# Performance work log

Measured on AMD Instinct MI355X. Metric: run time of the kernel, lower is better.

Reference implementation:

```python
import jax, jax.numpy as jnp
import numpy as np

EMBED_DIM = 768
NUM_HEADS = 12
HEAD_DIM = EMBED_DIM // NUM_HEADS


def setup_inputs() -> dict:
    key = jax.random.key(0)
    ks = jax.random.split(key, 12)
    B, T, D, Hp, Wp = 4, 32, EMBED_DIM, 16, 16
    h = jax.random.normal(ks[0], (B, T, D, Hp, Wp), dtype=jnp.float32)
    u_enc = jax.random.uniform(ks[1], (B, T, D, Hp, Wp), dtype=jnp.float32)
    lam = jax.random.uniform(ks[2], (B, T, 1, Hp, Wp), dtype=jnp.float32)
    s = 1.0 / np.sqrt(D)
    Wq = jax.random.normal(ks[3], (D, D), dtype=jnp.float32) * s
    bq = jnp.zeros((D,), dtype=jnp.float32)
    Wk = jax.random.normal(ks[4], (D, D), dtype=jnp.float32) * s
    bk = jnp.zeros((D,), dtype=jnp.float32)
    Wv = jax.random.normal(ks[5], (D, D), dtype=jnp.float32) * s
    bv = jnp.zeros((D,), dtype=jnp.float32)
    Wo = jax.random.normal(ks[6], (D, D), dtype=jnp.float32) * s
    bo = jnp.zeros((D,), dtype=jnp.float32)
    return {"h": h, "u_enc": u_enc, "lam": lam,
            "Wq": Wq, "bq": bq, "Wk": Wk, "bk": bk,
            "Wv": Wv, "bv": bv, "Wo": Wo, "bo": bo}


def reference(h, u_enc, lam, Wq, bq, Wk, bk, Wv, bv, Wo, bo):
    B, T, D, Hp, Wp = h.shape
    S = Hp * Wp
    NH, HD = NUM_HEADS, HEAD_DIM
    # (B,T,D,Hp,Wp) -> (B*S, T, D)
    h_seq = jnp.transpose(h, (0, 3, 4, 1, 2)).reshape(B * S, T, D)
    u_seq = jnp.transpose(u_enc, (0, 3, 4, 1, 2)).reshape(B * S, T, D)
    lam_seq = jnp.transpose(lam, (0, 3, 4, 1, 2)).reshape(B * S, T)
    # projections (nn.Linear: x @ W.T + b)
    Q = (h_seq @ Wq.T + bq).reshape(B * S, T, NH, HD).transpose(0, 2, 1, 3)
    K = (h_seq @ Wk.T + bk).reshape(B * S, T, NH, HD).transpose(0, 2, 1, 3)
    V = (h_seq @ Wv.T + bv).reshape(B * S, T, NH, HD).transpose(0, 2, 1, 3)
    scores = jnp.einsum('bhqd,bhkd->bhqk', Q, K) / jnp.sqrt(jnp.float32(HD))
    # key-dependent uncertainty penalty: lam_j * mean_d(u_j)
    u_pen = lam_seq * u_seq.mean(axis=-1)  # (B*S, T)
    scores = scores - u_pen[:, None, None, :]
    attn = jax.nn.softmax(scores, axis=-1)  # dropout: eval mode (identity)
    out = jnp.einsum('bhqk,bhkd->bhqd', attn, V)
    out = out.transpose(0, 2, 1, 3).reshape(B * S, T, D)
    out = out @ Wo.T + bo
    return jnp.transpose(out.reshape(B, Hp, Wp, T, D), (0, 3, 4, 1, 2))
```

## Files before the change

### kernel.cpp

```cpp
#include <hip/hip_runtime.h>

typedef float   f32x4 __attribute__((ext_vector_type(4)));
typedef _Float16 f16x8 __attribute__((ext_vector_type(8)));

#define DEV static __device__ __forceinline__

#define BB 4
#define TT 32
#define DD 768
#define SS 256
#define NHD 12
#define HD 64
#define NSEQ  (BB*SS)
#define MTOK  (NSEQ*TT)

DEV void async_copy16(const _Float16* g, _Float16* l) {
  __builtin_amdgcn_global_load_lds(
      (const __attribute__((address_space(1))) unsigned int*)g,
      (__attribute__((address_space(3))) unsigned int*)l,
      16, 0, 0);
}

DEV int swz_chunk(int r, int kc) {
  return r * 4 + (kc ^ (r & 3) ^ ((r >> 2) & 3));
}

__global__ __launch_bounds__(256) void k_transpose_h(const float* __restrict__ h,
                                                     _Float16* __restrict__ A) {
  __shared__ _Float16 Tl[256 * 65];
  const int slab = blockIdx.x;
  const int d0   = blockIdx.y * 64;
  const int t    = threadIdx.x;
  const float4* hv = (const float4*)(h + (slab * DD + d0) * SS);
  #pragma unroll
  for (int i = 0; i < 16; ++i) {
    int dd = i * 4 + (t >> 6);
    int s4 = (t & 63) * 4;
    float4 v = hv[dd * 64 + (t & 63)];
    Tl[(s4 + 0) * 65 + dd] = (_Float16)v.x;
    Tl[(s4 + 1) * 65 + dd] = (_Float16)v.y;
    Tl[(s4 + 2) * 65 + dd] = (_Float16)v.z;
    Tl[(s4 + 3) * 65 + dd] = (_Float16)v.w;
  }
  __syncthreads();
  #pragma unroll
  for (int p = 0; p < 8; ++p) {
    int s  = p * 32 + (t >> 3);
    int dd = (t & 7) * 8;
    f16x8 val;
    #pragma unroll
    for (int j = 0; j < 8; ++j) val[j] = Tl[s * 65 + dd + j];
    *(f16x8*)(A + (slab * SS + s) * DD + d0 + dd) = val;
  }
}

__global__ __launch_bounds__(256) void k_convert_w(const float* __restrict__ Wq,
                                                   const float* __restrict__ Wk,
                                                   const float* __restrict__ Wv,
                                                   const float* __restrict__ Wo,
                                                   _Float16* __restrict__ WQKV,
                                                   _Float16* __restrict__ WoH) {
  int idx = blockIdx.x * 256 + threadIdx.x;
  int row = idx / 96;
  int c8  = (idx % 96) * 8;
  const float* src; _Float16* dst;
  if (row < 768)       { src = Wq + row * 768;          dst = WQKV + row * 768; }
  else if (row < 1536) { src = Wk + (row - 768) * 768;  dst = WQKV + row * 768; }
  else if (row < 2304) { src = Wv + (row - 1536) * 768; dst = WQKV + row * 768; }
  else                 { src = Wo + (row - 2304) * 768; dst = WoH  + (row - 2304) * 768; }
  float4 v0 = *(const float4*)(src + c8);
  float4 v1 = *(const float4*)(src + c8 + 4);
  f16x8 o;
  o[0]=(_Float16)v0.x; o[1]=(_Float16)v0.y; o[2]=(_Float16)v0.z; o[3]=(_Float16)v0.w;
  o[4]=(_Float16)v1.x; o[5]=(_Float16)v1.y; o[6]=(_Float16)v1.z; o[7]=(_Float16)v1.w;
  *(f16x8*)(dst + c8) = o;
}

__global__ __launch_bounds__(256) void k_upen(const float* __restrict__ u,
                                              const float* __restrict__ lam,
                                              float* __restrict__ upen) {
  int slab = blockIdx.x >> 2;
  int q    = blockIdx.x & 3;
  int s    = threadIdx.x;
  const float* base = u + (slab * DD + q * 192) * SS + s;
  float sum = 0.f;
  for (int d = 0; d < 192; ++d) sum += base[d * SS];
  int b = slab >> 5, tt = slab & 31;
  float l = lam[slab * SS + s];
  atomicAdd(&upen[(b * SS + s) * TT + tt], sum * l * (1.0f / 768.0f));
}

__global__ __launch_bounds__(512, 2) void k_gemm_qkv(const _Float16* __restrict__ A,
                                                     const _Float16* __restrict__ Bw,
                                                     const float* __restrict__ bq,
                                                     const float* __restrict__ bk,
                                                     const float* __restrict__ bv,
                                                     _Float16* __restrict__ Qp,
                                                     _Float16* __restrict__ Kp,
                                                     _Float16* __restrict__ Vp) {
  __shared__ __align__(16) _Float16 As[2][256 * 64];
  __shared__ __align__(16) _Float16 Bs[2][256 * 64];
  const int swz = (blockIdx.x & 7) * 144 + (blockIdx.x >> 3);
  const int mt = swz / 9, nt = swz - mt * 9;
  const int m0 = mt * 256, n0 = nt * 256;
  const int tid = threadIdx.x, lane = tid & 63, w = tid >> 6;
  const int wm = w >> 2, wn = w & 3;
  f32x4 acc[8][4] = {};

  auto stage = [&](const _Float16* __restrict__ g, int grow0, _Float16* l, int k0) {
    #pragma unroll
    for (int li = 0; li < 4; ++li) {
      int cc = tid + 512 * li;
      int row = cc >> 3;
      int kc = (cc & 7) ^ (row & 7);
      async_copy16(g + (grow0 + row) * DD + k0 + kc * 8, l + cc * 8);
    }
  };

  stage(A, m0, &As[0][0], 0);
  stage(Bw, n0, &Bs[0][0], 0);
  __syncthreads();

  for (int it = 0; it < 12; ++it) {
    const int cb = it & 1;
    const _Float16* Ac = &As[cb][0];
    const _Float16* Bc = &Bs[cb][0];
    const int kn = (it + 1) * 64;
    f16x8 bfr[4][2];
    #pragma unroll
    for (int p = 0; p < 4; ++p) {
      f16x8 afr[2][2];
      #pragma unroll
      for (int q = 0; q < 2; ++q)
        #pragma unroll
        for (int kk = 0; kk < 2; ++kk) {
          int row = wm * 128 + (2 * p + q) * 16 + (lane & 15);
          int kc = kk * 4 + (lane >> 4);
          afr[q][kk] = *(const f16x8*)&Ac[row * 64 + (kc ^ (row & 7)) * 8];
        }
      if (p == 0) {
        #pragma unroll
        for (int ni = 0; ni < 4; ++ni)
          #pragma unroll
          for (int kk = 0; kk < 2; ++kk) {
            int row = wn * 64 + ni * 16 + (lane & 15);
            int kc = kk * 4 + (lane >> 4);
            bfr[ni][kk] = *(const f16x8*)&Bc[row * 64 + (kc ^ (row & 7)) * 8];
          }
        if (it < 11) stage(A, m0, &As[cb ^ 1][0], kn);
      }
      if (p == 1 && it < 11) stage(Bw, n0, &Bs[cb ^ 1][0], kn);
      __builtin_amdgcn_s_barrier();
      asm volatile("s_waitcnt lgkmcnt(0)" ::: "memory");
      __builtin_amdgcn_sched_barrier(0);
      __builtin_amdgcn_s_setprio(1);
      #pragma unroll
      for (int q = 0; q < 2; ++q)
        #pragma unroll
        for (int ni = 0; ni < 4; ++ni) {
          acc[2 * p + q][ni] = __builtin_amdgcn_mfma_f32_16x16x32_f16(
              afr[q][0], bfr[ni][0], acc[2 * p + q][ni], 0, 0, 0);
          acc[2 * p + q][ni] = __builtin_amdgcn_mfma_f32_16x16x32_f16(
              afr[q][1], bfr[ni][1], acc[2 * p + q][ni], 0, 0, 0);
        }
      __builtin_amdgcn_s_setprio(0);
      __builtin_amdgcn_s_barrier();
    }
    asm volatile("s_waitcnt vmcnt(0)" ::: "memory");
    __builtin_amdgcn_sched_barrier(0);
    __builtin_amdgcn_s_barrier();
  }

  const int sel = nt / 3;
  const float scale = (sel == 0) ? 0.125f : 1.0f;
  const float* bias = (sel == 0) ? bq : ((sel == 1) ? bk : bv);
  _Float16* dst = (sel == 0) ? Qp : ((sel == 1) ? Kp : Vp);
  const int b = mt >> 5, t = mt & 31;
  #pragma unroll
  for (int ni = 0; ni < 4; ++ni) {
    int n768 = nt * 256 - sel * 768 + wn * 64 + ni * 16 + (lane & 15);
    int head = n768 >> 6, hd = n768 & 63;
    float bs = bias[n768];
    long hb = (long)head * 2048 + t * 64 + hd;
    #pragma unroll
    for (int mi = 0; mi < 8; ++mi) {
      f32x4 v = acc[mi][ni];
      #pragma unroll
      for (int r = 0; r < 4; ++r) {
        int s = wm * 128 + mi * 16 + (lane >> 4) * 4 + r;
        long seq = (long)b * 256 + s;
        dst[seq * 24576 + hb] = (_Float16)((v[r] + bs) * scale);
      }
    }
  }
}

__global__ __launch_bounds__(256) void k_attn(const _Float16* __restrict__ Qp,
                                              const _Float16* __restrict__ Kp,
                                              const _Float16* __restrict__ Vp,
                                              const float* __restrict__ upen,
                                              _Float16* __restrict__ O) {
  __shared__ _Float16 lds[4][32 * 66 + 32 * 40];
  const int w = threadIdx.x >> 6, lane = threadIdx.x & 63;
  const int seq = blockIdx.x / 3, hg = blockIdx.x % 3;
  const int head = hg * 4 + w;
  const int b = seq >> 8, s = seq & 255;
  _Float16* Vs = &lds[w][0];
  _Float16* Ps = &lds[w][32 * 66];
  const long base = (long)(seq * NHD + head) * 2048;
  const _Float16* Qb = Qp + base;
  const _Float16* Kb = Kp + base;
  const _Float16* Vb = Vp + base;

  {
    int t = lane & 31, hh = (lane >> 5) * 32;
    f16x8 vc[4];
    #pragma unroll
    for (int c = 0; c < 4; ++c) vc[c] = *(const f16x8*)(Vb + t * 64 + hh + c * 8);
    #pragma unroll
    for (int c = 0; c < 4; ++c)
      #pragma unroll
      for (int p = 0; p < 4; ++p) {
        union { _Float16 h[2]; unsigned u; } pk;
        pk.h[0] = vc[c][2 * p]; pk.h[1] = vc[c][2 * p + 1];
        *(unsigned*)&Vs[t * 66 + hh + c * 8 + 2 * p] = pk.u;
      }
  }
  f16x8 qf[2][2], kf[2][2];
  #pragma unroll
  for (int i = 0; i < 2; ++i)
    #pragma unroll
    for (int ks = 0; ks < 2; ++ks) {
      int off = (i * 16 + (lane & 15)) * 64 + ks * 32 + (lane >> 4) * 8;
      qf[i][ks] = *(const f16x8*)(Qb + off);
      kf[i][ks] = *(const f16x8*)(Kb + off);
    }
  f32x4 sc[2][2] = {};
  #pragma unroll
  for (int mq = 0; mq < 2; ++mq)
    #pragma unroll
    for (int nk = 0; nk < 2; ++nk)
      #pragma unroll
      for (int ks = 0; ks < 2; ++ks)
        sc[mq][nk] = __builtin_amdgcn_mfma_f32_16x16x32_f16(qf[mq][ks], kf[nk][ks], sc[mq][nk], 0, 0, 0);

  const float up0 = upen[seq * TT + (lane & 15)];
  const float up1 = upen[seq * TT + 16 + (lane & 15)];

  #pragma unroll
  for (int mq = 0; mq < 2; ++mq) {
    #pragma unroll
    for (int r = 0; r < 4; ++r) {
      float s0 = sc[mq][0][r] - up0;
      float s1 = sc[mq][1][r] - up1;
      float mx = fmaxf(s0, s1);
      #pragma unroll
      for (int off = 1; off < 16; off <<= 1) mx = fmaxf(mx, __shfl_xor(mx, off, 64));
      float e0 = __expf(s0 - mx), e1 = __expf(s1 - mx);
      float sum = e0 + e1;
      #pragma unroll
      for (int off = 1; off < 16; off <<= 1) sum += __shfl_xor(sum, off, 64);
      float inv = 1.0f / sum;
      int row = mq * 16 + (lane >> 4) * 4 + r;
      Ps[row * 40 + (lane & 15)]      = (_Float16)(e0 * inv);
      Ps[row * 40 + 16 + (lane & 15)] = (_Float16)(e1 * inv);
    }
  }
  f16x8 pf[2];
  #pragma unroll
  for (int mq = 0; mq < 2; ++mq)
    pf[mq] = *(const f16x8*)(Ps + (mq * 16 + (lane & 15)) * 40 + (lane >> 4) * 8);
  f32x4 oacc[2][4] = {};
  #pragma unroll
  for (int nh = 0; nh < 4; ++nh) {
    int hd = nh * 16 + (lane & 15);
    f16x8 vf;
    #pragma unroll
    for (int j = 0; j < 8; ++j) vf[j] = Vs[((lane >> 4) * 8 + j) * 66 + hd];
    #pragma unroll
    for (int mq = 0; mq < 2; ++mq)
      oacc[mq][nh] = __builtin_amdgcn_mfma_f32_16x16x32_f16(pf[mq], vf, oacc[mq][nh], 0, 0, 0);
  }
  #pragma unroll
  for (int mq = 0; mq < 2; ++mq)
    #pragma unroll
    for (int nh = 0; nh < 4; ++nh) {
      int hd = nh * 16 + (lane & 15);
      #pragma unroll
      for (int r = 0; r < 4; ++r) {
        int t = mq * 16 + (lane >> 4) * 4 + r;
        O[((long)((b << 5) + t) * SS + s) * DD + head * HD + hd] = (_Float16)oacc[mq][nh][r];
      }
    }
}

__global__ __launch_bounds__(256, 2) void k_gemm_out(const _Float16* __restrict__ Wn,
                                                     const _Float16* __restrict__ O,
                                                     const float* __restrict__ bo,
                                                     float* __restrict__ out) {
  __shared__ _Float16 As[128 * 32];
  __shared__ _Float16 Bs[256 * 32];
  const int ct = blockIdx.x & 127, rt = blockIdx.x >> 7;
  const int R0 = rt * 128, C0 = ct * 256;
  const int tid = threadIdx.x, w = tid >> 6, lane = tid & 63;
  const int wr = (w >> 1) * 64, wcc = (w & 1) * 128;
  f32x4 acc[4][8] = {};
  for (int it = 0; it < 24; ++it) {
    const int k0 = it * 32;
    __syncthreads();
    #pragma unroll
    for (int i = 0; i < 2; ++i) {
      int c = tid + 256 * i;
      int row = c >> 2;
      int coff = ((c & 3) ^ (row & 3) ^ ((row >> 2) & 3)) * 8;
      _Float16* ldsA = (_Float16*)((char*)As + (w * 1024 + i * 4096 + lane * 16));
      async_copy16(Wn + (R0 + row) * DD + k0 + coff, ldsA);
    }
    #pragma unroll
    for (int i = 0; i < 4; ++i) {
      int c = tid + 256 * i;
      int row = c >> 2;
      int coff = ((c & 3) ^ (row & 3) ^ ((row >> 2) & 3)) * 8;
      _Float16* ldsB = (_Float16*)((char*)Bs + (w * 1024 + i * 4096 + lane * 16));
      async_copy16(O + (C0 + row) * DD + k0 + coff, ldsB);
    }
    __syncthreads();
    f16x8 af[4], bf[8];
    #pragma unroll
    for (int ri = 0; ri < 4; ++ri)
      af[ri] = *(const f16x8*)&As[swz_chunk(wr + ri * 16 + (lane & 15), lane >> 4) * 8];
    #pragma unroll
    for (int ci = 0; ci < 8; ++ci)
      bf[ci] = *(const f16x8*)&Bs[swz_chunk(wcc + ci * 16 + (lane & 15), lane >> 4) * 8];
    #pragma unroll
    for (int ri = 0; ri < 4; ++ri)
      #pragma unroll
      for (int ci = 0; ci < 8; ++ci)
        acc[ri][ci] = __builtin_amdgcn_mfma_f32_16x16x32_f16(af[ri], bf[ci], acc[ri][ci], 0, 0, 0);
  }
  const int slab = ct;
  #pragma unroll
  for (int ri = 0; ri < 4; ++ri) {
    #pragma unroll
    for (int ci = 0; ci < 8; ++ci) {
      int s = wcc + ci * 16 + (lane & 15);
      f32x4 v = acc[ri][ci];
      #pragma unroll
      for (int r = 0; r < 4; ++r) {
        int R = R0 + wr + ri * 16 + (lane >> 4) * 4 + r;
        out[((long)slab * DD + R) * SS + s] = v[r] + bo[R];
      }
    }
  }
}

extern "C" void kernel_launch(void* const* d_in, const int* in_sizes, int n_in,
                              void* d_out, int out_size, void* d_ws, size_t ws_size,
                              hipStream_t stream) {
  const float* h   = (const float*)d_in[0];
  const float* u   = (const float*)d_in[1];
  const float* lam = (const float*)d_in[2];
  const float* Wq  = (const float*)d_in[3];
  const float* bq  = (const float*)d_in[4];
  const float* Wk  = (const float*)d_in[5];
  const float* bk  = (const float*)d_in[6];
  const float* Wv  = (const float*)d_in[7];
  const float* bv  = (const float*)d_in[8];
  const float* Wo  = (const float*)d_in[9];
  const float* bo  = (const float*)d_in[10];
  float* out = (float*)d_out;

  char* ws = (char*)d_ws;
  _Float16* Abuf = (_Float16*)(ws);
  _Float16* WQKV = (_Float16*)(ws + 50331648);
  _Float16* WoH  = (_Float16*)(ws + 53870592);
  float*    upen = (float*)   (ws + 55050240);
  _Float16* Qp   = (_Float16*)(ws + 55181312);
  _Float16* Kp   = (_Float16*)(ws + 105512960);
  _Float16* Vp   = (_Float16*)(ws + 155844608);

  hipMemsetAsync(upen, 0, 32768 * sizeof(float), stream);
  k_transpose_h<<<dim3(128, 12), 256, 0, stream>>>(h, Abuf);
  k_convert_w<<<1152, 256, 0, stream>>>(Wq, Wk, Wv, Wo, WQKV, WoH);
  k_upen<<<512, 256, 0, stream>>>(u, lam, upen);
  k_gemm_qkv<<<1152, 512, 0, stream>>>(Abuf, WQKV, bq, bk, bv, Qp, Kp, Vp);
  k_attn<<<1024 * 3, 256, 0, stream>>>(Qp, Kp, Vp, upen, Abuf);
  k_gemm_out<<<128 * 6, 256, 0, stream>>>(WoH, Abuf, bo, out);
}
```

Before: 532.8 us.

## Deepen QKV GEMM pipeline to 4-stage K=32 ring buffer with 3 tiles in flight

Restructures the QKV projection GEMM main loop from a double-buffered K=64 scheme into a 4-slot ring of K=32 tiles, keeping three tiles of global-to-LDS async loads in flight. It uses vmcnt-based partial waits instead of draining all loads each iteration. The aim is to hide global memory latency better behind MFMA work. The cost is more barriers per unit of K and a different swizzle, and the counted waits must match the number of issued loads.

```diff
diff --git a/kernel.cpp b/kernel.cpp
--- a/kernel.cpp
+++ b/kernel.cpp
@@ -90,6 +90,43 @@
   atomicAdd(&upen[(b * SS + s) * TT + tt], sum * l * (1.0f / 768.0f));
 }
 
+#define KSTEP(IT, VM, DO_STG)                                                  \
+  {                                                                            \
+    const int bt_ = (IT) & 3;                                                  \
+    const _Float16* Ac = &As[bt_][0];                                          \
+    const _Float16* Bc = &Bs[bt_][0];                                          \
+    f16x8 af[8], bf[4];                                                        \
+    _Pragma("unroll")                                                          \
+    for (int mi = 0; mi < 8; ++mi) {                                           \
+      int row = wm * 128 + mi * 16 + (lane & 15);                              \
+      af[mi] = *(const f16x8*)&Ac[(row * 4 + ((lane >> 4) ^ (row & 3))) * 8];  \
+    }                                                                          \
+    _Pragma("unroll")                                                          \
+    for (int ni = 0; ni < 4; ++ni) {                                           \
+      int row = wn * 64 + ni * 16 + (lane & 15);                               \
+      bf[ni] = *(const f16x8*)&Bc[(row * 4 + ((lane >> 4) ^ (row & 3))) * 8];  \
+    }                                                                          \
+    if (DO_STG) {                                                              \
+      const int kn_ = ((IT) + 3) * 32;                                         \
+      stage(A, m0, &As[((IT) + 3) & 3][0], kn_);                               \
+      stage(Bw, n0, &Bs[((IT) + 3) & 3][0], kn_);                              \
+    }                                                                          \
+    __builtin_amdgcn_s_barrier();                                              \
+    asm volatile("s_waitcnt lgkmcnt(0)" ::: "memory");                         \
+    __builtin_amdgcn_sched_barrier(0);                                         \
+    __builtin_amdgcn_s_setprio(1);                                             \
+    _Pragma("unroll")                                                          \
+    for (int mi = 0; mi < 8; ++mi)                                             \
+      _Pragma("unroll")                                                        \
+      for (int ni = 0; ni < 4; ++ni)                                           \
+        acc[mi][ni] = __builtin_amdgcn_mfma_f32_16x16x32_f16(af[mi], bf[ni],   \
+                                                             acc[mi][ni], 0, 0, 0); \
+    __builtin_amdgcn_s_setprio(0);                                             \
+    asm volatile("s_waitcnt " VM ::: "memory");                                \
+    __builtin_amdgcn_sched_barrier(0);                                         \
+    __builtin_amdgcn_s_barrier();                                              \
+  }
+
 __global__ __launch_bounds__(512, 2) void k_gemm_qkv(const _Float16* __restrict__ A,
                                                      const _Float16* __restrict__ Bw,
                                                      const float* __restrict__ bq,
@@ -98,8 +135,8 @@
                                                      _Float16* __restrict__ Qp,
                                                      _Float16* __restrict__ Kp,
                                                      _Float16* __restrict__ Vp) {
-  __shared__ __align__(16) _Float16 As[2][256 * 64];
-  __shared__ __align__(16) _Float16 Bs[2][256 * 64];
+  __shared__ __align__(16) _Float16 As[4][256 * 32];
+  __shared__ __align__(16) _Float16 Bs[4][256 * 32];
   const int swz = (blockIdx.x & 7) * 144 + (blockIdx.x >> 3);
   const int mt = swz / 9, nt = swz - mt * 9;
   const int m0 = mt * 256, n0 = nt * 256;
@@ -109,67 +146,25 @@
 
   auto stage = [&](const _Float16* __restrict__ g, int grow0, _Float16* l, int k0) {
     #pragma unroll
-    for (int li = 0; li < 4; ++li) {
+    for (int li = 0; li < 2; ++li) {
       int cc = tid + 512 * li;
-      int row = cc >> 3;
-      int kc = (cc & 7) ^ (row & 7);
+      int row = cc >> 2;
+      int kc = (cc & 3) ^ (row & 3);
       async_copy16(g + (grow0 + row) * DD + k0 + kc * 8, l + cc * 8);
     }
   };
 
-  stage(A, m0, &As[0][0], 0);
-  stage(Bw, n0, &Bs[0][0], 0);
-  __syncthreads();
-
-  for (int it = 0; it < 12; ++it) {
-    const int cb = it & 1;
-    const _Float16* Ac = &As[cb][0];
-    const _Float16* Bc = &Bs[cb][0];
-    const int kn = (it + 1) * 64;
-    f16x8 bfr[4][2];
-    #pragma unroll
-    for (int p = 0; p < 4; ++p) {
-      f16x8 afr[2][2];
-      #pragma unroll
-      for (int q = 0; q < 2; ++q)
-        #pragma unroll
-        for (int kk = 0; kk < 2; ++kk) {
-          int row = wm * 128 + (2 * p + q) * 16 + (lane & 15);
-          int kc = kk * 4 + (lane >> 4);
-          afr[q][kk] = *(const f16x8*)&Ac[row * 64 + (kc ^ (row & 7)) * 8];
-        }
-      if (p == 0) {
-        #pragma unroll
-        for (int ni = 0; ni < 4; ++ni)
-          #pragma unroll
-          for (int kk = 0; kk < 2; ++kk) {
-            int row = wn * 64 + ni * 16 + (lane & 15);
-            int kc = kk * 4 + (lane >> 4);
-            bfr[ni][kk] = *(const f16x8*)&Bc[row * 64 + (kc ^ (row & 7)) * 8];
-          }
-        if (it < 11) stage(A, m0, &As[cb ^ 1][0], kn);
-      }
-      if (p == 1 && it < 11) stage(Bw, n0, &Bs[cb ^ 1][0], kn);
-      __builtin_amdgcn_s_barrier();
-      asm volatile("s_waitcnt lgkmcnt(0)" ::: "memory");
-      __builtin_amdgcn_sched_barrier(0);
-      __builtin_amdgcn_s_setprio(1);
-      #pragma unroll
-      for (int q = 0; q < 2; ++q)
-        #pragma unroll
-        for (int ni = 0; ni < 4; ++ni) {
-          acc[2 * p + q][ni] = __builtin_amdgcn_mfma_f32_16x16x32_f16(
-              afr[q][0], bfr[ni][0], acc[2 * p + q][ni], 0, 0, 0);
-          acc[2 * p + q][ni] = __builtin_amdgcn_mfma_f32_16x16x32_f16(
-              afr[q][1], bfr[ni][1], acc[2 * p + q][ni], 0, 0, 0);
-        }
-      __builtin_amdgcn_s_setprio(0);
-      __builtin_amdgcn_s_barrier();
-    }
-    asm volatile("s_waitcnt vmcnt(0)" ::: "memory");
-    __builtin_amdgcn_sched_barrier(0);
-    __builtin_amdgcn_s_barrier();
-  }
+  stage(A, m0, &As[0][0], 0);  stage(Bw, n0, &Bs[0][0], 0);
+  stage(A, m0, &As[1][0], 32); stage(Bw, n0, &Bs[1][0], 32);
+  stage(A, m0, &As[2][0], 64); stage(Bw, n0, &Bs[2][0], 64);
+  asm volatile("s_waitcnt vmcnt(8)" ::: "memory");
+  __builtin_amdgcn_sched_barrier(0);
+  __builtin_amdgcn_s_barrier();
+
+  for (int it = 0; it < 21; ++it) KSTEP(it, "vmcnt(8)", 1);
+  KSTEP(21, "vmcnt(4)", 0);
+  KSTEP(22, "vmcnt(0)", 0);
+  KSTEP(23, "vmcnt(0)", 0);
 
   const int sel = nt / 3;
   const float scale = (sel == 0) ? 0.125f : 1.0f;
```

New measurement: 535.3 us. No clear change (+0.5%).
